# Performance work log

Measured on AMD Instinct MI355X. Metric: run time of the kernel, lower is better.

Reference implementation:

```python
import jax, jax.numpy as jnp
import numpy as np

BLOCK_SIZE = 256

def setup_inputs() -> dict:
    key = jax.random.key(0)
    ks = jax.random.split(key, 5)
    B, T, C, H = 256, 256, 512, 64
    return {
        "x": jax.random.normal(ks[0], (B, T, C), dtype=jnp.float32),
        "y": jax.random.normal(ks[1], (B, T, C), dtype=jnp.float32),
        "Wq": jax.random.normal(ks[2], (C, H), dtype=jnp.float32) * (C ** -0.5),
        "Wk": jax.random.normal(ks[3], (C, H), dtype=jnp.float32) * (C ** -0.5),
        "Wv": jax.random.normal(ks[4], (C, H), dtype=jnp.float32) * (C ** -0.5),
    }

def reference(x, y, Wq, Wk, Wv):
    # q/k/v projections (Linear without bias): [B,T,C] @ [C,H] -> [B,T,H]
    q = jnp.einsum('btc,ch->bth', x, Wq)
    k = jnp.einsum('btc,ch->bth', y, Wk)
    v = jnp.einsum('btc,ch->bth', y, Wv)
    head_size = k.shape[-1]
    # scaled dot-product scores: [B,T,T]
    wei = jnp.einsum('bth,bsh->bts', q, k) * (head_size ** -0.5)
    # causal mask (is_causal=True): lower-triangular allowed
    T = x.shape[1]
    causal = jnp.tril(jnp.ones((T, T), dtype=bool))
    wei = jnp.where(causal, wei, -jnp.inf)
    wei = jax.nn.softmax(wei, axis=-1)
    # dropout omitted (eval mode / identity)
    out = jnp.einsum('bts,bsh->bth', wei, v)
    return out
```

## Files before the change

kernel.cpp:

```cpp
#include <hip/hip_runtime.h>


typedef _Float16 half8 __attribute__((ext_vector_type(8)));
typedef float floatx4 __attribute__((ext_vector_type(4)));

#define MFMA16(a, b, c) __builtin_amdgcn_mfma_f32_16x16x32_f16((a), (b), (c), 0, 0, 0)

__device__ inline half8 cvt8(float4 a, float4 b) {
  half8 r;
  r[0] = (_Float16)a.x; r[1] = (_Float16)a.y; r[2] = (_Float16)a.z; r[3] = (_Float16)a.w;
  r[4] = (_Float16)b.x; r[5] = (_Float16)b.y; r[6] = (_Float16)b.z; r[7] = (_Float16)b.w;
  return r;
}

template <int NOUT>
__global__ __launch_bounds__(256) void proj_kernel(
    const float* __restrict__ X, const float* __restrict__ W0,
    const float* __restrict__ W1, _Float16* __restrict__ O0,
    _Float16* __restrict__ O1t) {
  __shared__ _Float16 a_lds[128][40];
  __shared__ _Float16 w_lds[NOUT][64][40];
  __shared__ _Float16 vt_tile[NOUT == 2 ? 64 : 1][NOUT == 2 ? 136 : 1];

  const int tid = threadIdx.x;
  const int row0 = blockIdx.x * 128;
  const int wv = tid >> 6;
  const int lane = tid & 63;
  const int l15 = lane & 15, quad = lane >> 4;

  floatx4 acc[2][4 * NOUT];
#pragma unroll
  for (int i = 0; i < 2; i++)
#pragma unroll
    for (int j = 0; j < 4 * NOUT; j++) acc[i][j] = (floatx4)0.f;

  const int arow = tid >> 1;
  const int ahalf = (tid & 1) * 16;
  const int wkk = tid >> 3;
  const int wn0 = (tid & 7) * 8;

  for (int k0 = 0; k0 < 512; k0 += 32) {
    {
      const float4* s4 = (const float4*)(X + (size_t)(row0 + arow) * 512 + k0 + ahalf);
      float4 f0 = s4[0], f1 = s4[1], f2 = s4[2], f3 = s4[3];
      *(half8*)&a_lds[arow][ahalf]     = cvt8(f0, f1);
      *(half8*)&a_lds[arow][ahalf + 8] = cvt8(f2, f3);
    }
#pragma unroll
    for (int wi = 0; wi < NOUT; wi++) {
      const float* wsrc = (wi ? W1 : W0) + (size_t)(k0 + wkk) * 64 + wn0;
      float4 g0 = ((const float4*)wsrc)[0];
      float4 g1 = ((const float4*)wsrc)[1];
      w_lds[wi][wn0 + 0][wkk] = (_Float16)g0.x;
      w_lds[wi][wn0 + 1][wkk] = (_Float16)g0.y;
      w_lds[wi][wn0 + 2][wkk] = (_Float16)g0.z;
      w_lds[wi][wn0 + 3][wkk] = (_Float16)g0.w;
      w_lds[wi][wn0 + 4][wkk] = (_Float16)g1.x;
      w_lds[wi][wn0 + 5][wkk] = (_Float16)g1.y;
      w_lds[wi][wn0 + 6][wkk] = (_Float16)g1.z;
      w_lds[wi][wn0 + 7][wkk] = (_Float16)g1.w;
    }
    __syncthreads();
    half8 af0 = *(const half8*)&a_lds[wv * 32 + l15][quad * 8];
    half8 af1 = *(const half8*)&a_lds[wv * 32 + 16 + l15][quad * 8];
#pragma unroll
    for (int wi = 0; wi < NOUT; wi++)
#pragma unroll
      for (int j = 0; j < 4; j++) {
        half8 bf = *(const half8*)&w_lds[wi][j * 16 + l15][quad * 8];
        acc[0][wi * 4 + j] = MFMA16(af0, bf, acc[0][wi * 4 + j]);
        acc[1][wi * 4 + j] = MFMA16(af1, bf, acc[1][wi * 4 + j]);
      }
    __syncthreads();
  }
#pragma unroll
  for (int i = 0; i < 2; i++)
#pragma unroll
    for (int j = 0; j < 4; j++)
#pragma unroll
      for (int r = 0; r < 4; r++) {
        int grow = row0 + wv * 32 + i * 16 + quad * 4 + r;
        O0[(size_t)grow * 64 + j * 16 + l15] = (_Float16)acc[i][j][r];
      }
  if constexpr (NOUT == 2) {
#pragma unroll
    for (int i = 0; i < 2; i++)
#pragma unroll
      for (int j = 0; j < 4; j++)
#pragma unroll
        for (int r = 0; r < 4; r++) {
          int tl = wv * 32 + i * 16 + quad * 4 + r;
          vt_tile[j * 16 + l15][tl] = (_Float16)acc[i][4 + j][r];
        }
    __syncthreads();
    const int b = row0 >> 8, t0 = row0 & 255;
    const int h = tid >> 2;
    const int seg = (tid & 3) * 32;
    _Float16* dst = O1t + ((size_t)b * 64 + h) * 256 + t0 + seg;
#pragma unroll
    for (int e = 0; e < 4; e++)
      *(half8*)(dst + e * 8) = *(const half8*)&vt_tile[h][seg + e * 8];
  }
}

__global__ __launch_bounds__(256) void attn_kernel(
    const _Float16* __restrict__ Qw, const _Float16* __restrict__ Kw,
    const _Float16* __restrict__ Vt, float* __restrict__ Out) {
  __shared__ _Float16 p_lds[4][16][72];

  const int qt = blockIdx.x, bb = blockIdx.y;
  const int tid = threadIdx.x;
  const int wv = tid >> 6;
  const int lane = tid & 63;
  const int l15 = lane & 15, quad = lane >> 4;
  const float SCALE = 0.125f * 1.4426950408889634f;
  const float NEG = -3.0e38f;

  const size_t qoff = ((size_t)bb * 256 + qt * 64 + wv * 16 + l15) * 64 + quad * 8;
  half8 qf0 = *(const half8*)(Qw + qoff);
  half8 qf1 = *(const half8*)(Qw + qoff + 32);

  floatx4 o[4];
#pragma unroll
  for (int t = 0; t < 4; t++) o[t] = (floatx4)0.f;
  float mrow[4], lrow[4];
#pragma unroll
  for (int r = 0; r < 4; r++) { mrow[r] = NEG; lrow[r] = 0.f; }

  const _Float16* Kb = Kw + (size_t)bb * 256 * 64;
  const _Float16* Vb = Vt + (size_t)bb * 64 * 256;

  for (int j = 0; j <= qt; j++) {
    floatx4 sacc[4];
#pragma unroll
    for (int t = 0; t < 4; t++) sacc[t] = (floatx4)0.f;
#pragma unroll
    for (int t = 0; t < 4; t++) {
      const _Float16* kp = Kb + (size_t)(j * 64 + t * 16 + l15) * 64 + quad * 8;
      half8 b0 = *(const half8*)kp;
      half8 b1 = *(const half8*)(kp + 32);
      sacc[t] = MFMA16(qf0, b0, sacc[t]);
      sacc[t] = MFMA16(qf1, b1, sacc[t]);
    }

    half8 vb[2][4];
#pragma unroll
    for (int ss = 0; ss < 2; ss++)
#pragma unroll
      for (int th = 0; th < 4; th++)
        vb[ss][th] = *(const half8*)(Vb + (size_t)(th * 16 + l15) * 256 +
                                     j * 64 + ss * 32 + quad * 8);

    float y[4][4];
#pragma unroll
    for (int t = 0; t < 4; t++)
#pragma unroll
      for (int r = 0; r < 4; r++) y[t][r] = sacc[t][r] * SCALE;
    if (j == qt) {
#pragma unroll
      for (int t = 0; t < 4; t++)
#pragma unroll
        for (int r = 0; r < 4; r++)
          if (t * 16 + l15 > wv * 16 + quad * 4 + r) y[t][r] = NEG;
    }

#pragma unroll
    for (int r = 0; r < 4; r++) {
      float mx = fmaxf(fmaxf(y[0][r], y[1][r]), fmaxf(y[2][r], y[3][r]));
#pragma unroll
      for (int off = 1; off < 16; off <<= 1) mx = fmaxf(mx, __shfl_xor(mx, off, 64));
      float mnew = fmaxf(mrow[r], mx);
      float al = exp2f(mrow[r] - mnew);
      mrow[r] = mnew;
      float rs = 0.f;
#pragma unroll
      for (int t = 0; t < 4; t++) {
        float p = exp2f(y[t][r] - mnew);
        y[t][r] = p;
        rs += p;
      }
#pragma unroll
      for (int off = 1; off < 16; off <<= 1) rs += __shfl_xor(rs, off, 64);
      lrow[r] = lrow[r] * al + rs;
      o[0][r] *= al; o[1][r] *= al; o[2][r] *= al; o[3][r] *= al;
    }

#pragma unroll
    for (int t = 0; t < 4; t++)
#pragma unroll
      for (int r = 0; r < 4; r++)
        p_lds[wv][quad * 4 + r][t * 16 + l15] = (_Float16)y[t][r];

#pragma unroll
    for (int ss = 0; ss < 2; ss++) {
      half8 pa = *(const half8*)&p_lds[wv][l15][ss * 32 + quad * 8];
#pragma unroll
      for (int th = 0; th < 4; th++) o[th] = MFMA16(pa, vb[ss][th], o[th]);
    }
  }

#pragma unroll
  for (int th = 0; th < 4; th++)
#pragma unroll
    for (int r = 0; r < 4; r++) {
      int grow = qt * 64 + wv * 16 + quad * 4 + r;
      Out[((size_t)bb * 256 + grow) * 64 + th * 16 + l15] = o[th][r] / lrow[r];
    }
}

extern "C" void kernel_launch(void* const* d_in, const int* in_sizes, int n_in,
                              void* d_out, int out_size, void* d_ws, size_t ws_size,
                              hipStream_t stream) {
  const float* x  = (const float*)d_in[0];
  const float* y  = (const float*)d_in[1];
  const float* Wq = (const float*)d_in[2];
  const float* Wk = (const float*)d_in[3];
  const float* Wv = (const float*)d_in[4];
  float* out = (float*)d_out;

  _Float16* qw = (_Float16*)d_ws;
  _Float16* kw = qw + (size_t)65536 * 64;
  _Float16* vt = kw + (size_t)65536 * 64;

  proj_kernel<1><<<512, 256, 0, stream>>>(x, Wq, nullptr, qw, nullptr);
  proj_kernel<2><<<512, 256, 0, stream>>>(y, Wk, Wv, kw, vt);
  attn_kernel<<<dim3(4, 256), 256, 0, stream>>>(qw, kw, vt, out);
}
```

Baseline: 328.8 us.

## Stage K/V tiles in LDS with register prefetch of next tile

```diff
diff --git a/kernel.cpp b/kernel.cpp
--- a/kernel.cpp
+++ b/kernel.cpp
@@ -106,6 +106,8 @@
 __global__ __launch_bounds__(256) void attn_kernel(
     const _Float16* __restrict__ Qw, const _Float16* __restrict__ Kw,
     const _Float16* __restrict__ Vt, float* __restrict__ Out) {
+  __shared__ _Float16 k_lds[64][72];
+  __shared__ _Float16 vt_lds[64][72];
   __shared__ _Float16 p_lds[4][16][72];
 
   const int qt = blockIdx.x, bb = blockIdx.y;
@@ -130,26 +132,41 @@
   const _Float16* Kb = Kw + (size_t)bb * 256 * 64;
   const _Float16* Vb = Vt + (size_t)bb * 64 * 256;
 
+  const int srow = tid >> 2;
+  const int sc = (tid & 3) * 16;
+
+  half8 kr0, kr1, vr0, vr1;
+  {
+    const half8* kp = (const half8*)(Kb + (size_t)srow * 64 + sc);
+    kr0 = kp[0]; kr1 = kp[1];
+    const half8* vp = (const half8*)(Vb + (size_t)srow * 256 + sc);
+    vr0 = vp[0]; vr1 = vp[1];
+  }
+
   for (int j = 0; j <= qt; j++) {
+    *(half8*)&k_lds[srow][sc]      = kr0;
+    *(half8*)&k_lds[srow][sc + 8]  = kr1;
+    *(half8*)&vt_lds[srow][sc]     = vr0;
+    *(half8*)&vt_lds[srow][sc + 8] = vr1;
+    __syncthreads();
+
+    if (j < qt) {
+      const half8* kp = (const half8*)(Kb + (size_t)((j + 1) * 64 + srow) * 64 + sc);
+      kr0 = kp[0]; kr1 = kp[1];
+      const half8* vp = (const half8*)(Vb + (size_t)srow * 256 + (j + 1) * 64 + sc);
+      vr0 = vp[0]; vr1 = vp[1];
+    }
+
     floatx4 sacc[4];
 #pragma unroll
     for (int t = 0; t < 4; t++) sacc[t] = (floatx4)0.f;
 #pragma unroll
     for (int t = 0; t < 4; t++) {
-      const _Float16* kp = Kb + (size_t)(j * 64 + t * 16 + l15) * 64 + quad * 8;
-      half8 b0 = *(const half8*)kp;
-      half8 b1 = *(const half8*)(kp + 32);
+      half8 b0 = *(const half8*)&k_lds[t * 16 + l15][quad * 8];
       sacc[t] = MFMA16(qf0, b0, sacc[t]);
+      half8 b1 = *(const half8*)&k_lds[t * 16 + l15][32 + quad * 8];
       sacc[t] = MFMA16(qf1, b1, sacc[t]);
     }
-
-    half8 vb[2][4];
-#pragma unroll
-    for (int ss = 0; ss < 2; ss++)
-#pragma unroll
-      for (int th = 0; th < 4; th++)
-        vb[ss][th] = *(const half8*)(Vb + (size_t)(th * 16 + l15) * 256 +
-                                     j * 64 + ss * 32 + quad * 8);
 
     float y[4][4];
 #pragma unroll
@@ -195,8 +212,12 @@
     for (int ss = 0; ss < 2; ss++) {
       half8 pa = *(const half8*)&p_lds[wv][l15][ss * 32 + quad * 8];
 #pragma unroll
-      for (int th = 0; th < 4; th++) o[th] = MFMA16(pa, vb[ss][th], o[th]);
-    }
+      for (int th = 0; th < 4; th++) {
+        half8 vbf = *(const half8*)&vt_lds[th * 16 + l15][ss * 32 + quad * 8];
+        o[th] = MFMA16(pa, vbf, o[th]);
+      }
+    }
+    __syncthreads();
   }
 
 #pragma unroll
```

Result: faster. 318.1 us (-3.3%).
